# Kernel optimization log

Measured on AMD Instinct MI355X. Metric: run time of the kernel, lower is better.

## Reference

```python
import jax, jax.numpy as jnp
import numpy as np

NG, NL, NCAM, NP, ED = 8, 4, 6, 7, 256  # groups, levels, cams, key points, embed dims
GD = ED // NG
FIX_SCALE = jnp.array([[0.0, 0.0, 0.0], [0.45, 0.0, 0.0], [-0.45, 0.0, 0.0],
                       [0.0, 0.45, 0.0], [0.0, -0.45, 0.0], [0.0, 0.0, 0.45],
                       [0.0, 0.0, -0.45]], dtype=jnp.float32)


def grid_sample_bilinear(feat, grid):
    """feat [N,C,H,W], grid [N,A,P,2] in [-1,1]; bilinear, zeros padding, align_corners=False."""
    N, C, H, W = feat.shape
    A, P = grid.shape[1], grid.shape[2]
    gx = (grid[..., 0] + 1.0) * (W * 0.5) - 0.5
    gy = (grid[..., 1] + 1.0) * (H * 0.5) - 0.5
    x0 = jnp.floor(gx)
    y0 = jnp.floor(gy)
    wx1 = gx - x0
    wy1 = gy - y0
    feat_flat = feat.reshape(N, C, H * W)

    def gather(xi, yi, w):
        valid = (xi >= 0) & (xi <= W - 1) & (yi >= 0) & (yi <= H - 1)
        xc = jnp.clip(xi, 0, W - 1).astype(jnp.int32)
        yc = jnp.clip(yi, 0, H - 1).astype(jnp.int32)
        idx = (yc * W + xc).reshape(N, 1, A * P)
        vals = jnp.take_along_axis(feat_flat, idx, axis=2)  # [N,C,A*P]
        return vals * (w * valid).reshape(N, 1, A * P)

    out = (gather(x0, y0, (1.0 - wx1) * (1.0 - wy1))
           + gather(x0 + 1.0, y0, wx1 * (1.0 - wy1))
           + gather(x0, y0 + 1.0, (1.0 - wx1) * wy1)
           + gather(x0 + 1.0, y0 + 1.0, wx1 * wy1))
    return out.reshape(N, C, A, P)


def _forward(instance_feature, anchor, anchor_embed, feat0, feat1, feat2, feat3,
             projection_mat, image_wh, w_fc, b_fc, w_out, b_out):
    B, A = anchor.shape[:2]
    # --- key point generation (box_code_size=8: size + yaw rotation + translation) ---
    size = jnp.exp(anchor[..., 3:6])[:, :, None, :]           # [B,A,1,3]
    kp = FIX_SCALE * size                                      # [B,A,7,3]
    sin, cos = anchor[..., 6], anchor[..., 7]
    z = jnp.zeros_like(cos)
    o = jnp.ones_like(cos)
    rot = jnp.stack([jnp.stack([cos, -sin, z], -1),
                     jnp.stack([sin, cos, z], -1),
                     jnp.stack([z, z, o], -1)], -2)            # [B,A,3,3]
    kp = jnp.einsum('baij,bapj->bapi', rot, kp) + anchor[..., None, 0:3]

    # --- attention weights: softmax over cams*levels*pts per group ---
    feature = instance_feature + anchor_embed
    w = feature @ w_fc.T + b_fc                                # [B,A,NG*NCAM*NL*NP]
    w = jax.nn.softmax(w.reshape(B, A, NCAM * NL * NP, NG), axis=2)
    w = w.reshape(B, A, NCAM, NL, NP, NG)

    # --- project key points to normalized image coords ---
    pts = jnp.concatenate([kp, jnp.ones_like(kp[..., :1])], -1)  # [B,A,7,4]
    p2d = jnp.einsum('bcij,bapj->bcapi', projection_mat, pts)[..., :3]
    xy = p2d[..., :2] / jnp.maximum(p2d[..., 2:3], 1e-5)
    xy = xy / jnp.maximum(image_wh[:, :, None, None], 1e-5)
    grid = (xy * 2.0 - 1.0).reshape(B * NCAM, A, NP, 2)

    # --- multilevel bilinear sampling ---
    levels = [feat0, feat1, feat2, feat3]
    sampled = jnp.stack([grid_sample_bilinear(f.reshape((B * NCAM,) + f.shape[2:]), grid)
                         for f in levels], axis=1)             # [B*Ncam,NL,C,A,P]
    feats = sampled.reshape(B, NCAM, NL, ED, A, NP).transpose(0, 4, 1, 2, 5, 3)  # [B,A,Ncam,NL,P,C]
    feats = feats.reshape(B, A, NCAM, NL, NP, NG, GD)

    # --- weighted fusion over cams, levels, then sum over key points ---
    fused = jnp.einsum('bacnpgd,bacnpg->bagd', feats, w).reshape(B, A, ED)
    return fused @ w_out.T + b_out


def setup_inputs() -> dict:
    ks = jax.random.split(jax.random.key(0), 13)
    B, A = 2, 900
    return {
        'instance_feature': jax.random.normal(ks[0], (B, A, ED), jnp.float32),
        'anchor': jax.random.normal(ks[1], (B, A, 8), jnp.float32),
        'anchor_embed': jax.random.normal(ks[2], (B, A, ED), jnp.float32),
        'feat0': jax.random.normal(ks[3], (B, NCAM, ED, 64, 176), jnp.float32),
        'feat1': jax.random.normal(ks[4], (B, NCAM, ED, 32, 88), jnp.float32),
        'feat2': jax.random.normal(ks[5], (B, NCAM, ED, 16, 44), jnp.float32),
        'feat3': jax.random.normal(ks[6], (B, NCAM, ED, 8, 22), jnp.float32),
        'projection_mat': jax.random.normal(ks[7], (B, NCAM, 4, 4), jnp.float32),
        'image_wh': jnp.ones((B, NCAM, 2), jnp.float32),
        'w_fc': jax.random.normal(ks[8], (NG * NCAM * NL * NP, ED), jnp.float32) * 0.02,
        'b_fc': jax.random.normal(ks[9], (NG * NCAM * NL * NP,), jnp.float32) * 0.02,
        'w_out': jax.random.normal(ks[10], (ED, ED), jnp.float32) * 0.02,
        'b_out': jax.random.normal(ks[11], (ED,), jnp.float32) * 0.02,
    }


def reference(instance_feature, anchor, anchor_embed, feat0, feat1, feat2, feat3,
              projection_mat, image_wh, w_fc, b_fc, w_out, b_out):
    return _forward(instance_feature, anchor, anchor_embed, feat0, feat1, feat2, feat3,
                    projection_mat, image_wh, w_fc, b_fc, w_out, b_out)
```

## Files before the change

kernel.cpp:

```cpp
#include <hip/hip_runtime.h>
#include <math.h>

constexpr int B = 2, A = 900, ED = 256, NG = 8, NCAM = 6, NL = 4, NP = 7;
constexpr int NJ = NG * NCAM * NL * NP;
constexpr int NBA = B * A;
constexpr int NE = NCAM * NL * NP;
constexpr int LDST = 260;
constexpr int SPLIT = 2;
constexpr int EHALF = NE / SPLIT;

constexpr int NTRB = 116 * B * NCAM;
constexpr int NFCJ = 6;
constexpr int NFCB = (NBA / 8) * NFCJ;

__constant__ float FIXS[NP][3] = {
  {0.f,0.f,0.f},{0.45f,0.f,0.f},{-0.45f,0.f,0.f},
  {0.f,0.45f,0.f},{0.f,-0.45f,0.f},{0.f,0.f,0.45f},{0.f,0.f,-0.45f}};

__constant__ int cH[NL]  = {64,32,16,8};
__constant__ int cW[NL]  = {176,88,44,22};
__constant__ int cHW[NL] = {11264,2816,704,176};
__constant__ long long cLOFF[NL] = {0LL, 0LL, 8650752LL, 10813440LL};

__global__ __launch_bounds__(256) void k_prep(
    const float* __restrict__ f1, const float* __restrict__ f2,
    const float* __restrict__ f3,
    const float* __restrict__ inst, const float* __restrict__ emb,
    const float* __restrict__ w_fc, const float* __restrict__ b_fc,
    float* __restrict__ tfeat, float* __restrict__ wraw, int ntr)
{
  __shared__ float smem[32 * LDST];
  const int bid = blockIdx.x;
  const int t   = threadIdx.x;

  if (bid < ntr) {
    const int bc = bid / 116;
    const int bx = bid % 116;
    int lvl, t0;
    if      (bx < 88)  { lvl = 1; t0 = 0; }
    else if (bx < 110) { lvl = 2; t0 = 88; }
    else               { lvl = 3; t0 = 110; }
    const int HW  = cHW[lvl];
    const int px0 = (bx - t0) * 32;
    const float* in = ((lvl==1)?f1:(lvl==2)?f2:f3) + (size_t)bc * ED * HW + px0;
    float* outp = tfeat + cLOFF[lvl] + ((size_t)bc * HW + px0) * ED;
    const int npx = min(32, HW - px0);

#pragma unroll
    for (int j = 0; j < 8; ++j) {
      const int px = 4 * j;
      if (px < npx) {
        const float4 v = *(const float4*)(in + (size_t)t * HW + px);
        smem[(px+0)*LDST + t] = v.x;
        smem[(px+1)*LDST + t] = v.y;
        smem[(px+2)*LDST + t] = v.z;
        smem[(px+3)*LDST + t] = v.w;
      }
    }
    __syncthreads();
    const int wv = t >> 6, l = t & 63;
    for (int px = wv; px < npx; px += 4) {
      const float4 v = *(const float4*)&smem[px*LDST + 4*l];
      *(float4*)(outp + (size_t)px * ED + 4*l) = v;
    }
  } else {
    const int fb = bid - ntr;
    const int a0 = (fb / NFCJ) * 8;
    const int j  = (fb % NFCJ) * 256 + t;
    float* fsh = smem;

    for (int i = t; i < 8 * ED; i += 256) {
      const int a = i >> 8, k = i & 255;
      const size_t idx = (size_t)(a0 + a) * ED + k;
      fsh[a*ED + k] = inst[idx] + emb[idx];
    }
    __syncthreads();

    if (j < NJ) {
      float acc[8] = {0.f,0.f,0.f,0.f,0.f,0.f,0.f,0.f};
      const float* wrow = w_fc + (size_t)j * ED;
      for (int k = 0; k < ED; k += 4) {
        const float4 w4 = *(const float4*)(wrow + k);
#pragma unroll
        for (int a = 0; a < 8; ++a)
          acc[a] += w4.x*fsh[a*ED + k]   + w4.y*fsh[a*ED + k+1]
                  + w4.z*fsh[a*ED + k+2] + w4.w*fsh[a*ED + k+3];
      }
      const float bj = b_fc[j];
#pragma unroll
      for (int a = 0; a < 8; ++a)
        wraw[(size_t)(a0+a)*NJ + j] = acc[a] + bj;
    }
  }
}

template<bool CL>
__global__ __launch_bounds__(256) void k_sample_h(
    const float* __restrict__ anchor, const float* __restrict__ proj,
    const float* __restrict__ wh, const float* __restrict__ wraw,
    const float* __restrict__ tfeat,
    const float* __restrict__ f0, const float* __restrict__ f1,
    const float* __restrict__ f2, const float* __restrict__ f3,
    float* __restrict__ fused)
{
  __shared__ float wsh[NJ];
  __shared__ float gridsh[NCAM][NP][2];
  __shared__ const float* cptr[EHALF][4];
  __shared__ float4 cwt[EHALF];
  __shared__ int2   cmeta[EHALF];
  __shared__ int wcnt[4];

  const int ba   = blockIdx.x;
  const int half = blockIdx.y;
  const int b    = ba / A;
  const int t    = threadIdx.x;

  for (int j = t; j < NJ; j += 256)
    wsh[(j & 7) * NE + (j >> 3)] = wraw[(size_t)ba*NJ + j];

  if (t < NCAM*NP) {
    const int c = t / NP, p = t % NP;
    const float* an = anchor + (size_t)ba * 8;
    const float sx = expf(an[3]), sy = expf(an[4]), sz = expf(an[5]);
    const float sn = an[6], cs = an[7];
    const float kx = FIXS[p][0]*sx, ky = FIXS[p][1]*sy, kz = FIXS[p][2]*sz;
    const float px = cs*kx - sn*ky + an[0];
    const float py = sn*kx + cs*ky + an[1];
    const float pz = kz + an[2];
    const float* P = proj + ((size_t)(b*NCAM + c))*16;
    const float X = P[0]*px + P[1]*py + P[2]*pz  + P[3];
    const float Y = P[4]*px + P[5]*py + P[6]*pz  + P[7];
    const float Z = P[8]*px + P[9]*py + P[10]*pz + P[11];
    const float zc  = fmaxf(Z, 1e-5f);
    const float whx = fmaxf(wh[(b*NCAM+c)*2+0], 1e-5f);
    const float why = fmaxf(wh[(b*NCAM+c)*2+1], 1e-5f);
    gridsh[c][p][0] = (X/zc/whx)*2.f - 1.f;
    gridsh[c][p][1] = (Y/zc/why)*2.f - 1.f;
  }
  __syncthreads();

  bool valid = false;
  int chstep = 0;
  float4 w4 = make_float4(0.f,0.f,0.f,0.f);
  const float *p00=nullptr, *p10=nullptr, *p01=nullptr, *p11=nullptr;
  const int e = half * EHALF + t;
  if (t < EHALF) {
    const int c = e / (NL*NP); const int r = e % (NL*NP);
    const int l = r / NP, p = r % NP;
    const int Wl = cW[l], Hl = cH[l], HWl = cHW[l];
    const float gx = (gridsh[c][p][0] + 1.f) * (Wl * 0.5f) - 0.5f;
    const float gy = (gridsh[c][p][1] + 1.f) * (Hl * 0.5f) - 0.5f;
    const float x0f = floorf(gx), y0f = floorf(gy);
    const bool vx0 = (x0f >=  0.f) & (x0f <= (float)(Wl-1));
    const bool vx1 = (x0f >= -1.f) & (x0f <= (float)(Wl-2));
    const bool vy0 = (y0f >=  0.f) & (y0f <= (float)(Hl-1));
    const bool vy1 = (y0f >= -1.f) & (y0f <= (float)(Hl-2));
    if (vx0|vx1|vy0|vy1) {
      const float wx1 = gx - x0f, wy1 = gy - y0f;
      const int x0 = (int)fmaxf(fminf(x0f,        (float)(Wl-1)), 0.f);
      const int x1 = (int)fmaxf(fminf(x0f + 1.f,  (float)(Wl-1)), 0.f);
      const int y0 = (int)fmaxf(fminf(y0f,        (float)(Hl-1)), 0.f);
      const int y1 = (int)fmaxf(fminf(y0f + 1.f,  (float)(Hl-1)), 0.f);
      w4 = make_float4((1.f-wx1)*(1.f-wy1)*(vx0&&vy0),
                       wx1*(1.f-wy1)*(vx1&&vy0),
                       (1.f-wx1)*wy1*(vx0&&vy1),
                       wx1*wy1*(vx1&&vy1));
      if (w4.x != 0.f || w4.y != 0.f || w4.z != 0.f || w4.w != 0.f) {
        const float* base;
        int estep;
        if (CL && l >= 1) {
          base = tfeat + cLOFF[l] + (size_t)(b*NCAM + c) * HWl * ED;
          estep = ED; chstep = 1;
        } else {
          const float* fp = (l==0)?f0:(l==1)?f1:(l==2)?f2:f3;
          base = fp + (size_t)(b*NCAM + c) * ED * HWl;
          estep = 1; chstep = HWl;
        }
        p00 = base + (size_t)(y0*Wl + x0) * estep;
        p10 = base + (size_t)(y0*Wl + x1) * estep;
        p01 = base + (size_t)(y1*Wl + x0) * estep;
        p11 = base + (size_t)(y1*Wl + x1) * estep;
        valid = true;
      }
    }
  }

  const unsigned long long mask = __ballot(valid);
  const int lane = t & 63, wv = t >> 6;
  if (lane == 0) wcnt[wv] = __popcll(mask);
  __syncthreads();
  int off = 0, nv = 0;
#pragma unroll
  for (int i = 0; i < 4; ++i) { if (i < wv) off += wcnt[i]; nv += wcnt[i]; }
  if (valid) {
    const int pos = off + __popcll(mask & ((1ull << lane) - 1ull));
    cptr[pos][0] = p00; cptr[pos][1] = p10; cptr[pos][2] = p01; cptr[pos][3] = p11;
    cwt[pos]   = w4;
    cmeta[pos] = make_int2(chstep, e);
  }

  {
    const int g = t >> 5, ln = t & 31;
    float* wg = wsh + g * NE;
    float m = -3.4e38f;
    for (int i = ln; i < NE; i += 32) m = fmaxf(m, wg[i]);
#pragma unroll
    for (int mk = 16; mk >= 1; mk >>= 1) m = fmaxf(m, __shfl_xor(m, mk));
    float s = 0.f;
    for (int i = ln; i < NE; i += 32) {
      const float ev = expf(wg[i] - m);
      wg[i] = ev;
      s += ev;
    }
#pragma unroll
    for (int mk = 16; mk >= 1; mk >>= 1) s += __shfl_xor(s, mk);
    const float inv = 1.f / s;
    for (int i = ln; i < NE; i += 32) wg[i] *= inv;
  }
  __syncthreads();

  float acc = 0.f;
  const int g = t >> 5;
#pragma unroll 4
  for (int i = 0; i < nv; ++i) {
    const int2 m = cmeta[i];
    const size_t toff = (size_t)t * m.x;
    const float4 w = cwt[i];
    const float aw = wsh[g*NE + m.y];
    const float v00 = cptr[i][0][toff];
    const float v10 = cptr[i][1][toff];
    const float v01 = cptr[i][2][toff];
    const float v11 = cptr[i][3][toff];
    acc += aw * (w.x*v00 + w.y*v10 + w.z*v01 + w.w*v11);
  }
  fused[((size_t)half * NBA + ba) * ED + t] = acc;
}

__global__ __launch_bounds__(256) void k_out(const float* __restrict__ fused,
    const float* __restrict__ w_out, const float* __restrict__ b_out,
    float* __restrict__ out)
{
  __shared__ float fsh[8][ED];
  const int a0 = blockIdx.x * 8;
  const int t = threadIdx.x;
#pragma unroll
  for (int k = 0; k < 8; ++k)
    fsh[k][t] = fused[(size_t)(a0+k)*ED + t]
              + fused[(size_t)NBA*ED + (size_t)(a0+k)*ED + t];
  __syncthreads();
  float acc[8] = {0.f,0.f,0.f,0.f,0.f,0.f,0.f,0.f};
  for (int i = 0; i < ED; i += 4) {
    const float4 w4 = *(const float4*)&w_out[(size_t)t*ED + i];
#pragma unroll
    for (int k = 0; k < 8; ++k) {
      const float4 fv = *(const float4*)&fsh[k][i];
      acc[k] += w4.x*fv.x + w4.y*fv.y + w4.z*fv.z + w4.w*fv.w;
    }
  }
  const float bo = b_out[t];
#pragma unroll
  for (int k = 0; k < 8; ++k) out[(size_t)(a0+k)*ED + t] = acc[k] + bo;
}

extern "C" void kernel_launch(void* const* d_in, const int* in_sizes, int n_in,
                              void* d_out, int out_size, void* d_ws, size_t ws_size,
                              hipStream_t stream) {
  const float* inst   = (const float*)d_in[0];
  const float* anchor = (const float*)d_in[1];
  const float* emb    = (const float*)d_in[2];
  const float* f0 = (const float*)d_in[3];
  const float* f1 = (const float*)d_in[4];
  const float* f2 = (const float*)d_in[5];
  const float* f3 = (const float*)d_in[6];
  const float* proj  = (const float*)d_in[7];
  const float* wh    = (const float*)d_in[8];
  const float* w_fc  = (const float*)d_in[9];
  const float* b_fc  = (const float*)d_in[10];
  const float* w_out = (const float*)d_in[11];
  const float* b_out = (const float*)d_in[12];
  float* out = (float*)d_out;
  float* ws  = (float*)d_ws;

  const size_t TFEAT = 11354112ULL;
  const size_t WRAW  = (size_t)NBA * NJ;
  const size_t FUSED = (size_t)SPLIT * NBA * ED;
  const bool tr = ws_size >= (TFEAT + WRAW + FUSED) * sizeof(float);

  float* tfeat  = ws;
  float* wraw   = tr ? (ws + TFEAT) : ws;
  float* fusedp = wraw + WRAW;

  const int ntr = tr ? NTRB : 0;

  k_prep<<<ntr + NFCB, 256, 0, stream>>>(f1, f2, f3, inst, emb, w_fc, b_fc,
                                         tfeat, wraw, ntr);

  if (tr)
    k_sample_h<true><<<dim3(NBA, SPLIT), 256, 0, stream>>>(anchor, proj, wh,
        wraw, tfeat, f0, f1, f2, f3, fusedp);
  else
    k_sample_h<false><<<dim3(NBA, SPLIT), 256, 0, stream>>>(anchor, proj, wh,
        wraw, tfeat, f0, f1, f2, f3, fusedp);

  k_out<<<NBA / 8, 256, 0, stream>>>(fusedp, w_out, b_out, out);
}
```

Before: 365.6 us.

## Interleave transpose and FC blocks in prep kernel with smaller tiles and 2-row FC

The transpose tile shrinks from 32 to 16 pixels, which doubles the number of transpose blocks. Each level's pixel count is now an exact multiple of the tile, so the bounds checks are gone. Transpose blocks are spread evenly through the grid among the FC blocks, which should balance the two kinds of work across compute units. The FC part now has each thread compute two output rows and read features from shared memory as float4. That reuses each feature load and cuts the FC block count in half, at the cost of 32 idle threads per block and more registers.

```diff
diff --git a/kernel.cpp b/kernel.cpp
--- a/kernel.cpp
+++ b/kernel.cpp
@@ -9,9 +9,10 @@
 constexpr int SPLIT = 2;
 constexpr int EHALF = NE / SPLIT;
 
-constexpr int NTRB = 116 * B * NCAM;
-constexpr int NFCJ = 6;
-constexpr int NFCB = (NBA / 8) * NFCJ;
+constexpr int TPB   = 231;
+constexpr int NTRB  = TPB * B * NCAM;
+constexpr int NFCJ  = 3;
+constexpr int NFCB  = (NBA / 8) * NFCJ;
 
 __constant__ float FIXS[NP][3] = {
   {0.f,0.f,0.f},{0.45f,0.f,0.f},{-0.45f,0.f,0.f},
@@ -29,44 +30,47 @@
     const float* __restrict__ w_fc, const float* __restrict__ b_fc,
     float* __restrict__ tfeat, float* __restrict__ wraw, int ntr)
 {
-  __shared__ float smem[32 * LDST];
+  __shared__ float smem[16 * LDST];
   const int bid = blockIdx.x;
   const int t   = threadIdx.x;
-
-  if (bid < ntr) {
-    const int bc = bid / 116;
-    const int bx = bid % 116;
+  const int TOT = gridDim.x;
+
+  const int trb = (int)((long long)bid * ntr / TOT);
+  const int trn = (int)((long long)(bid + 1) * ntr / TOT);
+
+  if (trn > trb) {
+    const int bc = trb / TPB;
+    const int bx = trb % TPB;
     int lvl, t0;
-    if      (bx < 88)  { lvl = 1; t0 = 0; }
-    else if (bx < 110) { lvl = 2; t0 = 88; }
-    else               { lvl = 3; t0 = 110; }
+    if      (bx < 176) { lvl = 1; t0 = 0; }
+    else if (bx < 220) { lvl = 2; t0 = 176; }
+    else               { lvl = 3; t0 = 220; }
     const int HW  = cHW[lvl];
-    const int px0 = (bx - t0) * 32;
+    const int px0 = (bx - t0) * 16;
     const float* in = ((lvl==1)?f1:(lvl==2)?f2:f3) + (size_t)bc * ED * HW + px0;
     float* outp = tfeat + cLOFF[lvl] + ((size_t)bc * HW + px0) * ED;
-    const int npx = min(32, HW - px0);
-
-#pragma unroll
-    for (int j = 0; j < 8; ++j) {
+
+#pragma unroll
+    for (int j = 0; j < 4; ++j) {
       const int px = 4 * j;
-      if (px < npx) {
-        const float4 v = *(const float4*)(in + (size_t)t * HW + px);
-        smem[(px+0)*LDST + t] = v.x;
-        smem[(px+1)*LDST + t] = v.y;
-        smem[(px+2)*LDST + t] = v.z;
-        smem[(px+3)*LDST + t] = v.w;
-      }
+      const float4 v = *(const float4*)(in + (size_t)t * HW + px);
+      smem[(px+0)*LDST + t] = v.x;
+      smem[(px+1)*LDST + t] = v.y;
+      smem[(px+2)*LDST + t] = v.z;
+      smem[(px+3)*LDST + t] = v.w;
     }
     __syncthreads();
     const int wv = t >> 6, l = t & 63;
-    for (int px = wv; px < npx; px += 4) {
+#pragma unroll
+    for (int i = 0; i < 4; ++i) {
+      const int px = wv + 4 * i;
       const float4 v = *(const float4*)&smem[px*LDST + 4*l];
       *(float4*)(outp + (size_t)px * ED + 4*l) = v;
     }
   } else {
-    const int fb = bid - ntr;
+    const int fb = bid - trn;
     const int a0 = (fb / NFCJ) * 8;
-    const int j  = (fb % NFCJ) * 256 + t;
+    const int j0 = (fb % NFCJ) * 448;
     float* fsh = smem;
 
     for (int i = t; i < 8 * ED; i += 256) {
@@ -76,20 +80,28 @@
     }
     __syncthreads();
 
-    if (j < NJ) {
-      float acc[8] = {0.f,0.f,0.f,0.f,0.f,0.f,0.f,0.f};
-      const float* wrow = w_fc + (size_t)j * ED;
+    if (t < 224) {
+      const int jA = j0 + t, jB = jA + 224;
+      float accA[8] = {0.f,0.f,0.f,0.f,0.f,0.f,0.f,0.f};
+      float accB[8] = {0.f,0.f,0.f,0.f,0.f,0.f,0.f,0.f};
+      const float* wrA = w_fc + (size_t)jA * ED;
+      const float* wrB = w_fc + (size_t)jB * ED;
       for (int k = 0; k < ED; k += 4) {
-        const float4 w4 = *(const float4*)(wrow + k);
-#pragma unroll
-        for (int a = 0; a < 8; ++a)
-          acc[a] += w4.x*fsh[a*ED + k]   + w4.y*fsh[a*ED + k+1]
-                  + w4.z*fsh[a*ED + k+2] + w4.w*fsh[a*ED + k+3];
+        const float4 wa = *(const float4*)(wrA + k);
+        const float4 wb = *(const float4*)(wrB + k);
+#pragma unroll
+        for (int a = 0; a < 8; ++a) {
+          const float4 fv = *(const float4*)&fsh[a*ED + k];
+          accA[a] += wa.x*fv.x + wa.y*fv.y + wa.z*fv.z + wa.w*fv.w;
+          accB[a] += wb.x*fv.x + wb.y*fv.y + wb.z*fv.z + wb.w*fv.w;
+        }
       }
-      const float bj = b_fc[j];
-#pragma unroll
-      for (int a = 0; a < 8; ++a)
-        wraw[(size_t)(a0+a)*NJ + j] = acc[a] + bj;
+      const float bjA = b_fc[jA], bjB = b_fc[jB];
+#pragma unroll
+      for (int a = 0; a < 8; ++a) {
+        wraw[(size_t)(a0+a)*NJ + jA] = accA[a] + bjA;
+        wraw[(size_t)(a0+a)*NJ + jB] = accB[a] + bjB;
+      }
     }
   }
 }
```

After: 407.7 us. 11.5% more time.
